# Kernel optimization log

Measured on AMD Instinct MI355X. Metric: run time of the kernel, lower is better.

## Reference

```python
import jax, jax.numpy as jnp
import numpy as np
from jax import lax

RADIUS = 0.1
K_LOCAL = 32
N_CENTROIDS = 2048


def farthest_point_sample(pos, m):
    # Greedy FPS, deterministic start at index 0 (torch version uses a random start).
    pos = lax.stop_gradient(pos)  # index selection is non-differentiable
    N = pos.shape[0]
    big = jnp.finfo(pos.dtype).max

    def step(carry, _):
        dist, current = carry
        d2 = jnp.sum((pos - pos[current]) ** 2, axis=-1)  # (N,)
        dist = jnp.minimum(dist, d2)
        nxt = jnp.argmax(dist).astype(jnp.int32)
        return (dist, nxt), current

    init = (jnp.full((N,), big, dtype=pos.dtype), jnp.int32(0))
    _, idx = lax.scan(step, init, None, length=m)
    return idx  # (m,) int32


def ball_query(pos, centers, radius, k):
    # (M, N) pairwise squared distances -- same dense form as the torch reference.
    d2 = jnp.sum((centers[:, None, :] - pos[None, :, :]) ** 2, axis=-1)
    within = d2 <= radius * radius
    big = jnp.finfo(d2.dtype).max
    masked = jnp.where(within, d2, big)
    _, idx = lax.top_k(-masked, k)              # k smallest distances
    valid = jnp.take_along_axis(within, idx, axis=1)
    fallback = jnp.broadcast_to(idx[:, :1], idx.shape)
    return jnp.where(valid, idx, fallback)      # (M, k) padded with first (nearest) idx


def setup_inputs() -> dict:
    key = jax.random.key(0)
    ks = jax.random.split(key, 5)
    N, C = 50000, 128
    scale = 1.0 / np.sqrt(C)
    return {
        "pos": jax.random.uniform(ks[0], (N, 3), dtype=jnp.float32),
        "feat_scalar": jax.random.normal(ks[1], (N, C, 1), dtype=jnp.float32),
        "feat_vector": jax.random.normal(ks[2], (N, C, 3), dtype=jnp.float32),
        "W_scalar": jax.random.normal(ks[3], (C, C), dtype=jnp.float32) * scale,
        "W_vector": jax.random.normal(ks[4], (C, C), dtype=jnp.float32) * scale,
        "b_scalar": jnp.zeros((C,), dtype=jnp.float32),
        "b_vector": jnp.zeros((C,), dtype=jnp.float32),
    }


def reference(pos, feat_scalar, feat_vector, W_scalar, W_vector, b_scalar, b_vector):
    M = min(N_CENTROIDS, pos.shape[0])
    cent_idx = farthest_point_sample(pos, M)          # (M,)
    centroids = pos[cent_idx]                         # (M, 3)
    nbr_idx = ball_query(pos, centroids, RADIUS, K_LOCAL)  # (M, k)

    def pool_mix(f, W, b):
        f_nbr = f[nbr_idx]                            # (M, k, C, d) gather
        f_pooled = jnp.max(f_nbr, axis=1)             # (M, C, d) max-pool over neighbors
        # ChannelMixer: linear mix across channel dim
        return jnp.einsum('mcd,co->mod', f_pooled, W) + b[None, :, None]

    out_scalar = pool_mix(feat_scalar, W_scalar, b_scalar)
    out_vector = pool_mix(feat_vector, W_vector, b_vector)
    return centroids, out_scalar, out_vector
```

## Files before the change

### kernel.cpp

```cpp
#include <hip/hip_runtime.h>
#include <float.h>

#define N_PTS   50000
#define M_CENT  2048
#define K_LOC   32
#define C_CH    128

typedef unsigned long long u64;
typedef unsigned int u32;

#define FPS_NB   14
#define FPS_NT   512
#define FPS_PPT  7
#define FPS_R    64
#define SLOT_U64 8

__global__ void init_ws_kernel(u64* __restrict__ slots) {
  int t = blockIdx.x * blockDim.x + threadIdx.x;
  if (t < FPS_R * FPS_NB * SLOT_U64) slots[t] = 0ull;
}

template <int CTRL>
__device__ __forceinline__ u32 dppmov_u(u32 v) {
  return (u32)__builtin_amdgcn_update_dpp((int)v, (int)v, CTRL, 0xf, 0xf, false);
}
template <int CTRL>
__device__ __forceinline__ float dppmov_f(float v) {
  return __int_as_float(
      __builtin_amdgcn_update_dpp(__float_as_int(v), __float_as_int(v),
                                  CTRL, 0xf, 0xf, false));
}
__device__ __forceinline__ float wave_max_f32(float v) {
  v = fmaxf(v, dppmov_f<0x111>(v));
  v = fmaxf(v, dppmov_f<0x112>(v));
  v = fmaxf(v, dppmov_f<0x114>(v));
  v = fmaxf(v, dppmov_f<0x118>(v));
  v = fmaxf(v, dppmov_f<0x142>(v));
  v = fmaxf(v, dppmov_f<0x143>(v));
  return __int_as_float(__builtin_amdgcn_readlane(__float_as_int(v), 63));
}
__device__ __forceinline__ u32 wave_max_u32(u32 v) {
  u32 t;
  t = dppmov_u<0x111>(v); v = v > t ? v : t;
  t = dppmov_u<0x112>(v); v = v > t ? v : t;
  t = dppmov_u<0x114>(v); v = v > t ? v : t;
  t = dppmov_u<0x118>(v); v = v > t ? v : t;
  t = dppmov_u<0x142>(v); v = v > t ? v : t;
  t = dppmov_u<0x143>(v); v = v > t ? v : t;
  return (u32)__builtin_amdgcn_readlane((int)v, 63);
}
__device__ __forceinline__ u32 wave_min_u32(u32 v) {
  u32 t;
  t = dppmov_u<0x111>(v); v = v < t ? v : t;
  t = dppmov_u<0x112>(v); v = v < t ? v : t;
  t = dppmov_u<0x114>(v); v = v < t ? v : t;
  t = dppmov_u<0x118>(v); v = v < t ? v : t;
  t = dppmov_u<0x142>(v); v = v < t ? v : t;
  t = dppmov_u<0x143>(v); v = v < t ? v : t;
  return (u32)__builtin_amdgcn_readlane((int)v, 63);
}

__global__ __launch_bounds__(FPS_NT) void fps_kernel(
    const float* __restrict__ pos,
    u64* __restrict__ slots,
    float* __restrict__ cent_out)
{
  const int lane = threadIdx.x & 63;
  const int wv   = threadIdx.x >> 6;
  const int blk  = blockIdx.x;
  const int w    = blk * (FPS_NT/64) + wv;

  float px[FPS_PPT], py[FPS_PPT], pz[FPS_PPT], dist[FPS_PPT];
#pragma unroll
  for (int j = 0; j < FPS_PPT; j++) {
    int n = (w * FPS_PPT + j) * 64 + lane;
    if (n < N_PTS) {
      px[j] = pos[3*n+0]; py[j] = pos[3*n+1]; pz[j] = pos[3*n+2];
      dist[j] = FLT_MAX;
    } else {
      px[j] = 0.f; py[j] = 0.f; pz[j] = 0.f; dist[j] = -1.f;
    }
  }

  __shared__ uint2 s_w[2][FPS_NT/64];
  __shared__ float s_bc[2][3];

  float cx = pos[0], cy = pos[1], cz = pos[2];

  for (int i = 0; i < M_CENT; i++) {
    if (blk == 0 && wv == 0 && lane == 0) {
      cent_out[3*i+0] = cx; cent_out[3*i+1] = cy; cent_out[3*i+2] = cz;
    }
    float lmax = -1.0f;
#pragma unroll
    for (int j = 0; j < FPS_PPT; j++) {
      int n = (w * FPS_PPT + j) * 64 + lane;
      if (n < N_PTS) {
        float dx = __fsub_rn(px[j], cx);
        float dy = __fsub_rn(py[j], cy);
        float dz = __fsub_rn(pz[j], cz);
        float d2 = __fadd_rn(__fadd_rn(__fmul_rn(dx,dx), __fmul_rn(dy,dy)),
                             __fmul_rn(dz,dz));
        float d  = fminf(dist[j], d2);
        dist[j] = d;
        lmax = fmaxf(lmax, d);
      }
    }
    float wmax = wave_max_f32(lmax);
    u32 li = 0xFFFFFFFFu;
#pragma unroll
    for (int j = 0; j < FPS_PPT; j++) {
      int n = (w * FPS_PPT + j) * 64 + lane;
      if (n < N_PTS && dist[j] == wmax) li = li < (u32)n ? li : (u32)n;
    }
    u32 widx = wave_min_u32(li);

    if (i == M_CENT - 1) break;

    if (lane == 0) s_w[i & 1][wv] = make_uint2(__float_as_uint(wmax), widx);
    __syncthreads();

    if (wv == 0) {
      uint2 kv = (lane < FPS_NT/64) ? s_w[i & 1][lane]
                                    : make_uint2(0u, 0xFFFFFFFFu);
      u32 bmaxb = wave_max_u32(kv.x);
      u32 bidx  = wave_min_u32(kv.x == bmaxb ? kv.y : 0xFFFFFFFFu);
      u64* row = slots + (size_t)(i & (FPS_R-1)) * (FPS_NB*SLOT_U64);
      if (lane == 0) {
        u64 key = ((u64)bmaxb << 32) | (u64)(0xFFFFFFFFu - bidx);
        __hip_atomic_store(&row[blk * SLOT_U64], key,
                           __ATOMIC_RELAXED, __HIP_MEMORY_SCOPE_AGENT);
        if (i >= 2)
          __hip_atomic_store(&slots[(size_t)((i-2) & (FPS_R-1)) * (FPS_NB*SLOT_U64)
                                    + blk * SLOT_U64],
                             0ull, __ATOMIC_RELAXED, __HIP_MEMORY_SCOPE_AGENT);
      }
      u64 got = (lane < FPS_NB) ? 0ull : 1ull;
      const u64* sl = row + lane * SLOT_U64;
      while (__ballot(got == 0ull)) {
        if (got == 0ull)
          got = __hip_atomic_load(sl, __ATOMIC_RELAXED, __HIP_MEMORY_SCOPE_AGENT);
      }
      u32 hi = (u32)(got >> 32), lo = (u32)got;
      u32 ic = 0xFFFFFFFFu - lo;
      float qx = 0.f, qy = 0.f, qz = 0.f;
      if (lane < FPS_NB) { qx = pos[3*ic]; qy = pos[3*ic+1]; qz = pos[3*ic+2]; }

      u32 H  = wave_max_u32(lane < FPS_NB ? hi : 0u);
      u32 LO = wave_max_u32((lane < FPS_NB && hi == H) ? lo : 0u);
      u64 msk = __ballot(lane < FPS_NB && hi == H && lo == LO);
      int L = __ffsll((long long)msk) - 1;
      float ncx = __int_as_float(__builtin_amdgcn_readlane(__float_as_int(qx), L));
      float ncy = __int_as_float(__builtin_amdgcn_readlane(__float_as_int(qy), L));
      float ncz = __int_as_float(__builtin_amdgcn_readlane(__float_as_int(qz), L));
      if (lane == 0) {
        s_bc[i & 1][0] = ncx; s_bc[i & 1][1] = ncy; s_bc[i & 1][2] = ncz;
      }
    }
    __syncthreads();
    cx = s_bc[i & 1][0]; cy = s_bc[i & 1][1]; cz = s_bc[i & 1][2];
  }
}

#define BQ_NT  256
#define BQ_CAP 2048

__global__ __launch_bounds__(BQ_NT) void ballq_kernel(
    const float* __restrict__ pos,
    const float* __restrict__ cent,
    int* __restrict__ nbr,
    int* __restrict__ nsel)
{
  __shared__ float s_d2[BQ_CAP];
  __shared__ int   s_idx[BQ_CAP];
  __shared__ int   s_count;
  __shared__ u64   s_red[BQ_NT/64];
  __shared__ u64   s_win;

  const int m = blockIdx.x, tid = threadIdx.x;
  if (tid == 0) s_count = 0;
  __syncthreads();
  const float cx = cent[3*m+0], cy = cent[3*m+1], cz = cent[3*m+2];

  for (int n = tid; n < N_PTS; n += BQ_NT) {
    float dx = __fsub_rn(cx, pos[3*n+0]);
    float dy = __fsub_rn(cy, pos[3*n+1]);
    float dz = __fsub_rn(cz, pos[3*n+2]);
    float d2 = __fadd_rn(__fadd_rn(__fmul_rn(dx,dx), __fmul_rn(dy,dy)),
                         __fmul_rn(dz,dz));
    if (d2 <= 0.01f) {
      int p = atomicAdd(&s_count, 1);
      if (p < BQ_CAP) { s_d2[p] = d2; s_idx[p] = n; }
    }
  }
  __syncthreads();
  int cnt = s_count; if (cnt > BQ_CAP) cnt = BQ_CAP;
  int ns = cnt < K_LOC ? cnt : K_LOC;

  for (int sel = 0; sel < ns; sel++) {
    u64 best = ~0ull;
    for (int p = tid; p < cnt; p += BQ_NT) {
      u64 pk = ((u64)__float_as_uint(s_d2[p]) << 32) | (u64)(u32)s_idx[p];
      if (pk < best) best = pk;
    }
#pragma unroll
    for (int off = 32; off >= 1; off >>= 1) {
      u64 o = __shfl_down(best, off, 64);
      if (o < best) best = o;
    }
    if ((tid & 63) == 0) s_red[tid >> 6] = best;
    __syncthreads();
    if (tid < 64) {
      best = (tid < BQ_NT/64) ? s_red[tid] : ~0ull;
#pragma unroll
      for (int off = 2; off >= 1; off >>= 1) {
        u64 o = __shfl_down(best, off, 64);
        if (o < best) best = o;
      }
      if (tid == 0) s_win = best;
    }
    __syncthreads();
    int widx = (int)(u32)(s_win & 0xFFFFFFFFull);
    if (tid == 0) nbr[m*K_LOC + sel] = widx;
    for (int p = tid; p < cnt; p += BQ_NT) {
      if (s_idx[p] == widx) s_d2[p] = FLT_MAX;
    }
    __syncthreads();
  }
  if (tid == 0) nsel[m] = ns;
}

__global__ __launch_bounds__(C_CH) void pool_mix_kernel(
    const float* __restrict__ fs,
    const float* __restrict__ fv,
    const float* __restrict__ Ws,
    const float* __restrict__ Wv,
    const float* __restrict__ bs,
    const float* __restrict__ bv,
    const int* __restrict__ nbr,
    const int* __restrict__ nsel,
    float* __restrict__ out_s,
    float* __restrict__ out_v)
{
  __shared__ float ps[C_CH];
  __shared__ float pv[C_CH*3];
  const int m = blockIdx.x, o = threadIdx.x;
  const int ns = nsel[m];
  float mS = -FLT_MAX, m0 = -FLT_MAX, m1 = -FLT_MAX, m2 = -FLT_MAX;
  for (int j = 0; j < ns; j++) {
    int n = nbr[m*K_LOC + j];
    mS = fmaxf(mS, fs[(size_t)n*C_CH + o]);
    const float* r = fv + (size_t)n*(C_CH*3) + 3*o;
    m0 = fmaxf(m0, r[0]); m1 = fmaxf(m1, r[1]); m2 = fmaxf(m2, r[2]);
  }
  ps[o] = mS; pv[3*o+0] = m0; pv[3*o+1] = m1; pv[3*o+2] = m2;
  __syncthreads();
  float aS = bs[o];
  float a0 = bv[o], a1 = bv[o], a2 = bv[o];
  for (int cc = 0; cc < C_CH; cc++) {
    float w1 = Ws[cc*C_CH + o];
    float w2 = Wv[cc*C_CH + o];
    aS = fmaf(ps[cc], w1, aS);
    a0 = fmaf(pv[3*cc+0], w2, a0);
    a1 = fmaf(pv[3*cc+1], w2, a1);
    a2 = fmaf(pv[3*cc+2], w2, a2);
  }
  out_s[(size_t)m*C_CH + o] = aS;
  float* ov = out_v + (size_t)m*(C_CH*3) + 3*o;
  ov[0] = a0; ov[1] = a1; ov[2] = a2;
}

extern "C" void kernel_launch(void* const* d_in, const int* in_sizes, int n_in,
                              void* d_out, int out_size, void* d_ws, size_t ws_size,
                              hipStream_t stream) {
  (void)in_sizes; (void)n_in; (void)out_size; (void)ws_size;
  const float* pos = (const float*)d_in[0];
  const float* fs  = (const float*)d_in[1];
  const float* fv  = (const float*)d_in[2];
  const float* Ws  = (const float*)d_in[3];
  const float* Wv  = (const float*)d_in[4];
  const float* bs  = (const float*)d_in[5];
  const float* bv  = (const float*)d_in[6];

  float* out      = (float*)d_out;
  float* cent_out = out;
  float* out_s    = out + 3*M_CENT;
  float* out_v    = out + 3*M_CENT + M_CENT*C_CH;

  char* ws = (char*)d_ws;
  u64* slots = (u64*)ws;
  size_t slots_bytes = (size_t)FPS_R * FPS_NB * SLOT_U64 * 8;
  int* nbr   = (int*)(ws + slots_bytes);
  int* nsel  = (int*)(ws + slots_bytes + (size_t)M_CENT*K_LOC*4);

  init_ws_kernel<<<(FPS_R*FPS_NB*SLOT_U64 + 255)/256, 256, 0, stream>>>(slots);
  fps_kernel<<<FPS_NB, FPS_NT, 0, stream>>>(pos, slots, cent_out);
  ballq_kernel<<<M_CENT, BQ_NT, 0, stream>>>(pos, cent_out, nbr, nsel);
  pool_mix_kernel<<<M_CENT, C_CH, 0, stream>>>(fs, fv, Ws, Wv, bs, bv,
                                               nbr, nsel, out_s, out_v);
}
```

Before: 4.078 ms.

## Co-locate FPS blocks on one XCC and poll slots via L2 atomics

Launches 128 blocks and uses per-XCC tickets so the first XCC to gather 14 blocks wins. Only those 14 run FPS, which keeps all inter-block slot traffic inside one XCC's L2. Because the blocks share an L2, slot loads and stores become non-coherent L2 atomics (atomic_or with sc0, atomic_swap) instead of agent-scope atomics, with a handshake that falls back to the safe path if the blocks cannot all see each other. This is meant to cut the per-iteration cross-block sync latency of the 2048-step FPS loop. In exchange it adds a startup handshake, a bounded-poll escape, and reliance on hardware-specific XCC_ID behaviour. The slot rows 61-63 that the handshake reuses overlap the ring buffer and are not cleared per iteration.

Measured after the change: 3.858 ms. -5.4%, faster.

```diff
diff --git a/kernel.cpp b/kernel.cpp
--- a/kernel.cpp
+++ b/kernel.cpp
@@ -9,15 +9,39 @@
 typedef unsigned long long u64;
 typedef unsigned int u32;
 
-#define FPS_NB   14
-#define FPS_NT   512
-#define FPS_PPT  7
-#define FPS_R    64
-#define SLOT_U64 8
+#define FPS_NB    14
+#define FPS_GRID  128
+#define FPS_NT    512
+#define FPS_PPT   7
+#define FPS_R     64
+#define SLOT_U64  8
+#define ROW_U64   (FPS_NB*SLOT_U64)
+#define FPS_POLL_BOUND (1<<16)
 
 __global__ void init_ws_kernel(u64* __restrict__ slots) {
   int t = blockIdx.x * blockDim.x + threadIdx.x;
   if (t < FPS_R * FPS_NB * SLOT_U64) slots[t] = 0ull;
+}
+
+__device__ __forceinline__ u64 l2a_load(u64* p) {
+  u64 old;
+  asm volatile("global_atomic_or_x2 %0, %1, %2, off sc0\n\ts_waitcnt vmcnt(0)"
+               : "=&v"(old) : "v"(p), "v"(0ull) : "memory");
+  return old;
+}
+__device__ __forceinline__ void l2a_store(u64* p, u64 v) {
+  asm volatile("global_atomic_swap_x2 %0, %1, off"
+               :: "v"(p), "v"(v) : "memory");
+}
+template <bool SAFE>
+__device__ __forceinline__ u64 slot_load(u64* p) {
+  if (SAFE) return __hip_atomic_load(p, __ATOMIC_RELAXED, __HIP_MEMORY_SCOPE_AGENT);
+  return l2a_load(p);
+}
+template <bool SAFE>
+__device__ __forceinline__ void slot_store(u64* p, u64 v) {
+  if (SAFE) __hip_atomic_store(p, v, __ATOMIC_RELAXED, __HIP_MEMORY_SCOPE_AGENT);
+  else      l2a_store(p, v);
 }
 
 template <int CTRL>
@@ -60,15 +84,15 @@
   return (u32)__builtin_amdgcn_readlane((int)v, 63);
 }
 
-__global__ __launch_bounds__(FPS_NT) void fps_kernel(
-    const float* __restrict__ pos,
-    u64* __restrict__ slots,
-    float* __restrict__ cent_out)
+template <bool SAFE>
+__device__ __forceinline__ void fps_main(
+    const float* __restrict__ pos, u64* __restrict__ slots,
+    float* __restrict__ cent_out, const int wid,
+    uint2 (*s_w)[FPS_NT/64], float (*s_bc)[3])
 {
   const int lane = threadIdx.x & 63;
   const int wv   = threadIdx.x >> 6;
-  const int blk  = blockIdx.x;
-  const int w    = blk * (FPS_NT/64) + wv;
+  const int w    = wid * (FPS_NT/64) + wv;
 
   float px[FPS_PPT], py[FPS_PPT], pz[FPS_PPT], dist[FPS_PPT];
 #pragma unroll
@@ -82,13 +106,12 @@
     }
   }
 
-  __shared__ uint2 s_w[2][FPS_NT/64];
-  __shared__ float s_bc[2][3];
+  bool broken = false;
 
   float cx = pos[0], cy = pos[1], cz = pos[2];
 
   for (int i = 0; i < M_CENT; i++) {
-    if (blk == 0 && wv == 0 && lane == 0) {
+    if (wid == 0 && wv == 0 && lane == 0) {
       cent_out[3*i+0] = cx; cent_out[3*i+1] = cy; cent_out[3*i+2] = cz;
     }
     float lmax = -1.0f;
@@ -125,24 +148,35 @@
                                     : make_uint2(0u, 0xFFFFFFFFu);
       u32 bmaxb = wave_max_u32(kv.x);
       u32 bidx  = wave_min_u32(kv.x == bmaxb ? kv.y : 0xFFFFFFFFu);
-      u64* row = slots + (size_t)(i & (FPS_R-1)) * (FPS_NB*SLOT_U64);
-      if (lane == 0) {
-        u64 key = ((u64)bmaxb << 32) | (u64)(0xFFFFFFFFu - bidx);
-        __hip_atomic_store(&row[blk * SLOT_U64], key,
-                           __ATOMIC_RELAXED, __HIP_MEMORY_SCOPE_AGENT);
-        if (i >= 2)
-          __hip_atomic_store(&slots[(size_t)((i-2) & (FPS_R-1)) * (FPS_NB*SLOT_U64)
-                                    + blk * SLOT_U64],
-                             0ull, __ATOMIC_RELAXED, __HIP_MEMORY_SCOPE_AGENT);
-      }
-      u64 got = (lane < FPS_NB) ? 0ull : 1ull;
-      const u64* sl = row + lane * SLOT_U64;
-      while (__ballot(got == 0ull)) {
-        if (got == 0ull)
-          got = __hip_atomic_load(sl, __ATOMIC_RELAXED, __HIP_MEMORY_SCOPE_AGENT);
+      u64 ownkey = ((u64)bmaxb << 32) | (u64)(0xFFFFFFFFu - bidx);
+      u64* row = slots + (size_t)(i & (FPS_R-1)) * ROW_U64;
+
+      u64 got;
+      if (!SAFE && broken) {
+        got = (lane == wid) ? ownkey : 1ull;
+      } else {
+        if (lane == 0) {
+          slot_store<SAFE>(&row[wid * SLOT_U64], ownkey);
+          if (i >= 2)
+            slot_store<SAFE>(&slots[(size_t)((i-2) & (FPS_R-1)) * ROW_U64
+                                    + wid * SLOT_U64], 0ull);
+        }
+        got = (lane < FPS_NB) ? 0ull : 1ull;
+        u64* sl = row + lane * SLOT_U64;
+        int trips = 0;
+        while (__ballot(got == 0ull)) {
+          if (got == 0ull) got = slot_load<SAFE>(sl);
+          if (!SAFE) {
+            if (++trips > FPS_POLL_BOUND) {
+              if (got == 0ull) got = 1ull;
+              broken = true;
+            }
+          }
+        }
       }
       u32 hi = (u32)(got >> 32), lo = (u32)got;
       u32 ic = 0xFFFFFFFFu - lo;
+      if (ic >= N_PTS) ic = 0;
       float qx = 0.f, qy = 0.f, qz = 0.f;
       if (lane < FPS_NB) { qx = pos[3*ic]; qy = pos[3*ic+1]; qz = pos[3*ic+2]; }
 
@@ -160,6 +194,72 @@
     __syncthreads();
     cx = s_bc[i & 1][0]; cy = s_bc[i & 1][1]; cz = s_bc[i & 1][2];
   }
+}
+
+__global__ __launch_bounds__(FPS_NT) void fps_kernel(
+    const float* __restrict__ pos,
+    u64* __restrict__ slots,
+    float* __restrict__ cent_out)
+{
+  __shared__ uint2 s_w[2][FPS_NT/64];
+  __shared__ float s_bc[2][3];
+  __shared__ int   s_role[2];
+
+  if (threadIdx.x == 0) {
+    u32 xcc;
+    asm volatile("s_getreg_b32 %0, hwreg(HW_REG_XCC_ID, 0, 4)" : "=s"(xcc));
+    xcc &= 7u;
+    u64* cntp = slots + 63*ROW_U64 + (size_t)xcc * SLOT_U64 + 1;
+    u64* winp = slots + 63*ROW_U64 + 8 * SLOT_U64 + 1;
+    u64 t = __hip_atomic_fetch_add(cntp, 1ull, __ATOMIC_RELAXED,
+                                   __HIP_MEMORY_SCOPE_AGENT);
+    int ticket = (int)t;
+    if (ticket == FPS_NB - 1) {
+      u64 exp = 0ull;
+      __hip_atomic_compare_exchange_strong(winp, &exp, (u64)(xcc + 1),
+          __ATOMIC_RELAXED, __ATOMIC_RELAXED, __HIP_MEMORY_SCOPE_AGENT);
+    }
+    int role = -1, safe = 0;
+    if (ticket < FPS_NB) {
+      u64 win;
+      do {
+        win = __hip_atomic_load(winp, __ATOMIC_RELAXED, __HIP_MEMORY_SCOPE_AGENT);
+        if (win == 0ull) __builtin_amdgcn_s_sleep(1);
+      } while (win == 0ull);
+      if (win == (u64)(xcc + 1)) {
+        role = ticket;
+        u64* hs = slots + 61*ROW_U64;
+        l2a_store(hs + (size_t)role * SLOT_U64 + 1, 1ull);
+        bool okk = false;
+        for (int trip = 0; trip < 512 && !okk; ++trip) {
+          int seen = 0;
+          for (int j = 0; j < FPS_NB; ++j)
+            seen += (l2a_load(hs + (size_t)j * SLOT_U64 + 1) != 0ull);
+          okk = (seen == FPS_NB);
+          if (!okk) __builtin_amdgcn_s_sleep(8);
+        }
+        u64* okp = slots + 62*ROW_U64;
+        __hip_atomic_store(okp + (size_t)role * SLOT_U64 + 1,
+                           okk ? 2ull : 1ull,
+                           __ATOMIC_RELAXED, __HIP_MEMORY_SCOPE_AGENT);
+        for (int j = 0; j < FPS_NB; ++j) {
+          u64 v;
+          do {
+            v = __hip_atomic_load(okp + (size_t)j * SLOT_U64 + 1,
+                                  __ATOMIC_RELAXED, __HIP_MEMORY_SCOPE_AGENT);
+            if (v == 0ull) __builtin_amdgcn_s_sleep(1);
+          } while (v == 0ull);
+          if (v == 1ull) safe = 1;
+        }
+      }
+    }
+    s_role[0] = role; s_role[1] = safe;
+  }
+  __syncthreads();
+  const int wid = s_role[0];
+  if (wid < 0) return;
+  if (s_role[1]) fps_main<true >(pos, slots, cent_out, wid, s_w, s_bc);
+  else           fps_main<false>(pos, slots, cent_out, wid, s_w, s_bc);
 }
 
 #define BQ_NT  256
@@ -294,7 +394,7 @@
   int* nsel  = (int*)(ws + slots_bytes + (size_t)M_CENT*K_LOC*4);
 
   init_ws_kernel<<<(FPS_R*FPS_NB*SLOT_U64 + 255)/256, 256, 0, stream>>>(slots);
-  fps_kernel<<<FPS_NB, FPS_NT, 0, stream>>>(pos, slots, cent_out);
+  fps_kernel<<<FPS_GRID, FPS_NT, 0, stream>>>(pos, slots, cent_out);
   ballq_kernel<<<M_CENT, BQ_NT, 0, stream>>>(pos, cent_out, nbr, nsel);
   pool_mix_kernel<<<M_CENT, C_CH, 0, stream>>>(fs, fv, Ws, Wv, bs, bv,
                                                nbr, nsel, out_s, out_v);
```

## Replace multi-block FPS with single-block grid-culled FPS using chunk bounding boxes

Applied to the files above, without the earlier changes.

Points are binned into a 10x10x10 grid and sorted into 64-point chunks, each with a bounding box. Farthest point sampling then runs in one 1024-thread block, which replaces the cross-block atomic slot handshake. Each iteration updates only the chunks whose box could still be lowered by the new centroid, since their cached max distance exceeds the lower bound. This cuts per-iteration distance work and global synchronization, at the cost of several preprocessing kernels, global-memory distance reads and writes, and running on a single CU.

After: 4.855 ms. 19.1% more time.

```diff
diff --git a/kernel.cpp b/kernel.cpp
--- a/kernel.cpp
+++ b/kernel.cpp
@@ -9,15 +9,21 @@
 typedef unsigned long long u64;
 typedef unsigned int u32;
 
-#define FPS_NB   14
-#define FPS_NT   512
-#define FPS_PPT  7
-#define FPS_R    64
-#define SLOT_U64 8
-
-__global__ void init_ws_kernel(u64* __restrict__ slots) {
-  int t = blockIdx.x * blockDim.x + threadIdx.x;
-  if (t < FPS_R * FPS_NB * SLOT_U64) slots[t] = 0ull;
+#define G_DIM   10
+#define N_CELL  (G_DIM*G_DIM*G_DIM)
+#define NC_MAX  2048
+#define NP_PAD  50176
+#define FPS1_NT 1024
+#define NWAVE   (FPS1_NT/64)
+
+__device__ __forceinline__ int cell_of(float x, float y, float z) {
+  int a = (int)(x * (float)G_DIM);
+  int b = (int)(y * (float)G_DIM);
+  int c = (int)(z * (float)G_DIM);
+  a = a < 0 ? 0 : (a > G_DIM-1 ? G_DIM-1 : a);
+  b = b < 0 ? 0 : (b > G_DIM-1 ? G_DIM-1 : b);
+  c = c < 0 ? 0 : (c > G_DIM-1 ? G_DIM-1 : c);
+  return (a * G_DIM + b) * G_DIM + c;
 }
 
 template <int CTRL>
@@ -39,126 +45,218 @@
   v = fmaxf(v, dppmov_f<0x143>(v));
   return __int_as_float(__builtin_amdgcn_readlane(__float_as_int(v), 63));
 }
-__device__ __forceinline__ u32 wave_max_u32(u32 v) {
-  u32 t;
-  t = dppmov_u<0x111>(v); v = v > t ? v : t;
-  t = dppmov_u<0x112>(v); v = v > t ? v : t;
-  t = dppmov_u<0x114>(v); v = v > t ? v : t;
-  t = dppmov_u<0x118>(v); v = v > t ? v : t;
-  t = dppmov_u<0x142>(v); v = v > t ? v : t;
-  t = dppmov_u<0x143>(v); v = v > t ? v : t;
-  return (u32)__builtin_amdgcn_readlane((int)v, 63);
-}
-__device__ __forceinline__ u32 wave_min_u32(u32 v) {
-  u32 t;
-  t = dppmov_u<0x111>(v); v = v < t ? v : t;
-  t = dppmov_u<0x112>(v); v = v < t ? v : t;
-  t = dppmov_u<0x114>(v); v = v < t ? v : t;
-  t = dppmov_u<0x118>(v); v = v < t ? v : t;
-  t = dppmov_u<0x142>(v); v = v < t ? v : t;
-  t = dppmov_u<0x143>(v); v = v < t ? v : t;
-  return (u32)__builtin_amdgcn_readlane((int)v, 63);
-}
-
-__global__ __launch_bounds__(FPS_NT) void fps_kernel(
+__device__ __forceinline__ float wave_min_f32(float v) {
+  v = fminf(v, dppmov_f<0x111>(v));
+  v = fminf(v, dppmov_f<0x112>(v));
+  v = fminf(v, dppmov_f<0x114>(v));
+  v = fminf(v, dppmov_f<0x118>(v));
+  v = fminf(v, dppmov_f<0x142>(v));
+  v = fminf(v, dppmov_f<0x143>(v));
+  return __int_as_float(__builtin_amdgcn_readlane(__float_as_int(v), 63));
+}
+template <int CTRL>
+__device__ __forceinline__ u64 dpp_u64(u64 v) {
+  u32 hi = dppmov_u<CTRL>((u32)(v >> 32));
+  u32 lo = dppmov_u<CTRL>((u32)v);
+  return ((u64)hi << 32) | (u64)lo;
+}
+__device__ __forceinline__ u64 wave_max_u64(u64 v) {
+  u64 t;
+  t = dpp_u64<0x111>(v); if (t > v) v = t;
+  t = dpp_u64<0x112>(v); if (t > v) v = t;
+  t = dpp_u64<0x114>(v); if (t > v) v = t;
+  t = dpp_u64<0x118>(v); if (t > v) v = t;
+  t = dpp_u64<0x142>(v); if (t > v) v = t;
+  t = dpp_u64<0x143>(v); if (t > v) v = t;
+  u32 rh = (u32)__builtin_amdgcn_readlane((int)(v >> 32), 63);
+  u32 rl = (u32)__builtin_amdgcn_readlane((int)(v & 0xFFFFFFFFull), 63);
+  return ((u64)rh << 32) | (u64)rl;
+}
+
+__global__ void init_zero_kernel(int* __restrict__ p, int n) {
+  int t = blockIdx.x * blockDim.x + threadIdx.x;
+  if (t < n) p[t] = 0;
+}
+
+__global__ void hist_kernel(const float* __restrict__ pos,
+                            int* __restrict__ cellcnt) {
+  int n = blockIdx.x * blockDim.x + threadIdx.x;
+  if (n >= N_PTS) return;
+  atomicAdd(&cellcnt[cell_of(pos[3*n], pos[3*n+1], pos[3*n+2])], 1);
+}
+
+__global__ __launch_bounds__(1024) void scan_kernel(
+    const int* __restrict__ cellcnt, int* __restrict__ cursor,
+    int2* __restrict__ rng, int* __restrict__ ncp)
+{
+  __shared__ int s[1024];
+  const int tid = threadIdx.x;
+  int cnt = (tid < N_CELL) ? cellcnt[tid] : 0;
+  s[tid] = cnt;
+  __syncthreads();
+  for (int off = 1; off < 1024; off <<= 1) {
+    int add = (tid >= off) ? s[tid - off] : 0;
+    __syncthreads();
+    s[tid] += add;
+    __syncthreads();
+  }
+  int pofs = s[tid] - cnt;
+  int nch  = (cnt + 63) >> 6;
+  __syncthreads();
+  s[tid] = nch;
+  __syncthreads();
+  for (int off = 1; off < 1024; off <<= 1) {
+    int add = (tid >= off) ? s[tid - off] : 0;
+    __syncthreads();
+    s[tid] += add;
+    __syncthreads();
+  }
+  int chbase = s[tid] - nch;
+  if (tid < N_CELL) {
+    cursor[tid] = pofs;
+    for (int k = 0; k < nch; k++) {
+      int rem = cnt - (k << 6);
+      rng[chbase + k] = make_int2(pofs + (k << 6), rem < 64 ? rem : 64);
+    }
+  }
+  if (tid == 1023) *ncp = s[1023];
+}
+
+__global__ void scatter_kernel(const float* __restrict__ pos,
+    int* __restrict__ cursor,
+    float* __restrict__ spx, float* __restrict__ spy,
+    float* __restrict__ spz, int* __restrict__ sidx)
+{
+  int n = blockIdx.x * blockDim.x + threadIdx.x;
+  if (n >= N_PTS) return;
+  float x = pos[3*n], y = pos[3*n+1], z = pos[3*n+2];
+  int p = atomicAdd(&cursor[cell_of(x, y, z)], 1);
+  spx[p] = x; spy[p] = y; spz[p] = z; sidx[p] = n;
+}
+
+__global__ __launch_bounds__(64) void bbox_kernel(
+    const float* __restrict__ spx, const float* __restrict__ spy,
+    const float* __restrict__ spz, const int2* __restrict__ rng,
+    const int* __restrict__ ncp,
+    float4* __restrict__ bb_lo, float4* __restrict__ bb_hi,
+    float* __restrict__ sdist)
+{
+  const int b = blockIdx.x, lane = threadIdx.x;
+  int gid = b * 64 + lane;
+  if (gid < N_PTS) sdist[gid] = FLT_MAX;
+  int NC = *ncp;
+  if (b >= NC) return;
+  int2 rc = rng[b];
+  bool v = lane < rc.y;
+  int g = rc.x + lane;
+  float x = v ? spx[g] : 0.f, y = v ? spy[g] : 0.f, z = v ? spz[g] : 0.f;
+  float lx = wave_min_f32(v ? x :  FLT_MAX);
+  float ly = wave_min_f32(v ? y :  FLT_MAX);
+  float lz = wave_min_f32(v ? z :  FLT_MAX);
+  float hx = wave_max_f32(v ? x : -FLT_MAX);
+  float hy = wave_max_f32(v ? y : -FLT_MAX);
+  float hz = wave_max_f32(v ? z : -FLT_MAX);
+  if (lane == 0) {
+    bb_lo[b] = make_float4(lx, ly, lz, 0.f);
+    bb_hi[b] = make_float4(hx, hy, hz, 0.f);
+  }
+}
+
+__global__ __launch_bounds__(FPS1_NT) void fps_kernel(
     const float* __restrict__ pos,
-    u64* __restrict__ slots,
-    float* __restrict__ cent_out)
-{
-  const int lane = threadIdx.x & 63;
-  const int wv   = threadIdx.x >> 6;
-  const int blk  = blockIdx.x;
-  const int w    = blk * (FPS_NT/64) + wv;
-
-  float px[FPS_PPT], py[FPS_PPT], pz[FPS_PPT], dist[FPS_PPT];
-#pragma unroll
-  for (int j = 0; j < FPS_PPT; j++) {
-    int n = (w * FPS_PPT + j) * 64 + lane;
-    if (n < N_PTS) {
-      px[j] = pos[3*n+0]; py[j] = pos[3*n+1]; pz[j] = pos[3*n+2];
-      dist[j] = FLT_MAX;
-    } else {
-      px[j] = 0.f; py[j] = 0.f; pz[j] = 0.f; dist[j] = -1.f;
-    }
-  }
-
-  __shared__ uint2 s_w[2][FPS_NT/64];
-  __shared__ float s_bc[2][3];
+    const float* __restrict__ spx, const float* __restrict__ spy,
+    const float* __restrict__ spz, const int* __restrict__ sidx,
+    float* __restrict__ sdist, const int2* __restrict__ rng,
+    const float4* __restrict__ bb_lo, const float4* __restrict__ bb_hi,
+    const int* __restrict__ ncp, float* __restrict__ cent_out)
+{
+  __shared__ u64  l_key[NC_MAX];
+  __shared__ int2 l_rng[NC_MAX];
+  __shared__ int  l_act[NC_MAX];
+  __shared__ u64  l_red[NWAVE];
+  __shared__ int  l_nact;
+  __shared__ u32  l_win;
+
+  const int tid = threadIdx.x, lane = tid & 63, wv = tid >> 6;
+  const int NC = *ncp;
+
+  for (int c = tid; c < NC; c += FPS1_NT) {
+    l_rng[c] = rng[c];
+    l_key[c] = ((u64)0x7F7FFFFFu) << 32;
+  }
+  __syncthreads();
 
   float cx = pos[0], cy = pos[1], cz = pos[2];
 
   for (int i = 0; i < M_CENT; i++) {
-    if (blk == 0 && wv == 0 && lane == 0) {
+    if (tid == 0) {
       cent_out[3*i+0] = cx; cent_out[3*i+1] = cy; cent_out[3*i+2] = cz;
-    }
-    float lmax = -1.0f;
-#pragma unroll
-    for (int j = 0; j < FPS_PPT; j++) {
-      int n = (w * FPS_PPT + j) * 64 + lane;
-      if (n < N_PTS) {
-        float dx = __fsub_rn(px[j], cx);
-        float dy = __fsub_rn(py[j], cy);
-        float dz = __fsub_rn(pz[j], cz);
-        float d2 = __fadd_rn(__fadd_rn(__fmul_rn(dx,dx), __fmul_rn(dy,dy)),
-                             __fmul_rn(dz,dz));
-        float d  = fminf(dist[j], d2);
-        dist[j] = d;
-        lmax = fmaxf(lmax, d);
+      l_nact = 0;
+    }
+    if (i == M_CENT - 1) break;
+    __syncthreads();
+
+    for (int c0 = 0; c0 < NC; c0 += FPS1_NT) {
+      int c = c0 + tid;
+      bool act = false;
+      if (c < NC) {
+        float cmax = __uint_as_float((u32)(l_key[c] >> 32));
+        float4 lo = bb_lo[c], hi = bb_hi[c];
+        float ax = fmaxf(fmaxf(__fsub_rn(lo.x, cx), __fsub_rn(cx, hi.x)), 0.f);
+        float ay = fmaxf(fmaxf(__fsub_rn(lo.y, cy), __fsub_rn(cy, hi.y)), 0.f);
+        float az = fmaxf(fmaxf(__fsub_rn(lo.z, cz), __fsub_rn(cz, hi.z)), 0.f);
+        float LB = (ax*ax + ay*ay + az*az) * 0.999f;
+        act = LB < cmax;
       }
-    }
-    float wmax = wave_max_f32(lmax);
-    u32 li = 0xFFFFFFFFu;
-#pragma unroll
-    for (int j = 0; j < FPS_PPT; j++) {
-      int n = (w * FPS_PPT + j) * 64 + lane;
-      if (n < N_PTS && dist[j] == wmax) li = li < (u32)n ? li : (u32)n;
-    }
-    u32 widx = wave_min_u32(li);
-
-    if (i == M_CENT - 1) break;
-
-    if (lane == 0) s_w[i & 1][wv] = make_uint2(__float_as_uint(wmax), widx);
-    __syncthreads();
-
+      u64 m = __ballot(act);
+      if (m) {
+        int leader = __ffsll((long long)m) - 1;
+        int base = 0;
+        if (lane == leader) base = atomicAdd(&l_nact, __popcll(m));
+        base = __shfl(base, leader, 64);
+        if (act)
+          l_act[base + __popcll(m & ((1ull << lane) - 1ull))] = c;
+      }
+    }
+    __syncthreads();
+
+    int nact = l_nact;
+    for (int a = wv; a < nact; a += NWAVE) {
+      int c = l_act[a];
+      int2 rc = l_rng[c];
+      u64 key = 0ull;
+      if (lane < rc.y) {
+        int g = rc.x + lane;
+        float dx = __fsub_rn(spx[g], cx);
+        float dy = __fsub_rn(spy[g], cy);
+        float dz = __fsub_rn(spz[g], cz);
+        float d2 = __fadd_rn(__fadd_rn(__fmul_rn(dx, dx), __fmul_rn(dy, dy)),
+                             __fmul_rn(dz, dz));
+        float d = fminf(sdist[g], d2);
+        sdist[g] = d;
+        key = ((u64)__float_as_uint(d) << 32) | (u64)(u32)(~(u32)sidx[g]);
+      }
+      key = wave_max_u64(key);
+      if (lane == 0) l_key[c] = key;
+    }
+    __syncthreads();
+
+    u64 best = 0ull;
+    for (int c = tid; c < NC; c += FPS1_NT) {
+      u64 k = l_key[c];
+      if (k > best) best = k;
+    }
+    best = wave_max_u64(best);
+    if (lane == 0) l_red[wv] = best;
+    __syncthreads();
     if (wv == 0) {
-      uint2 kv = (lane < FPS_NT/64) ? s_w[i & 1][lane]
-                                    : make_uint2(0u, 0xFFFFFFFFu);
-      u32 bmaxb = wave_max_u32(kv.x);
-      u32 bidx  = wave_min_u32(kv.x == bmaxb ? kv.y : 0xFFFFFFFFu);
-      u64* row = slots + (size_t)(i & (FPS_R-1)) * (FPS_NB*SLOT_U64);
-      if (lane == 0) {
-        u64 key = ((u64)bmaxb << 32) | (u64)(0xFFFFFFFFu - bidx);
-        __hip_atomic_store(&row[blk * SLOT_U64], key,
-                           __ATOMIC_RELAXED, __HIP_MEMORY_SCOPE_AGENT);
-        if (i >= 2)
-          __hip_atomic_store(&slots[(size_t)((i-2) & (FPS_R-1)) * (FPS_NB*SLOT_U64)
-                                    + blk * SLOT_U64],
-                             0ull, __ATOMIC_RELAXED, __HIP_MEMORY_SCOPE_AGENT);
-      }
-      u64 got = (lane < FPS_NB) ? 0ull : 1ull;
-      const u64* sl = row + lane * SLOT_U64;
-      while (__ballot(got == 0ull)) {
-        if (got == 0ull)
-          got = __hip_atomic_load(sl, __ATOMIC_RELAXED, __HIP_MEMORY_SCOPE_AGENT);
-      }
-      u32 hi = (u32)(got >> 32), lo = (u32)got;
-      u32 ic = 0xFFFFFFFFu - lo;
-      float qx = 0.f, qy = 0.f, qz = 0.f;
-      if (lane < FPS_NB) { qx = pos[3*ic]; qy = pos[3*ic+1]; qz = pos[3*ic+2]; }
-
-      u32 H  = wave_max_u32(lane < FPS_NB ? hi : 0u);
-      u32 LO = wave_max_u32((lane < FPS_NB && hi == H) ? lo : 0u);
-      u64 msk = __ballot(lane < FPS_NB && hi == H && lo == LO);
-      int L = __ffsll((long long)msk) - 1;
-      float ncx = __int_as_float(__builtin_amdgcn_readlane(__float_as_int(qx), L));
-      float ncy = __int_as_float(__builtin_amdgcn_readlane(__float_as_int(qy), L));
-      float ncz = __int_as_float(__builtin_amdgcn_readlane(__float_as_int(qz), L));
-      if (lane == 0) {
-        s_bc[i & 1][0] = ncx; s_bc[i & 1][1] = ncy; s_bc[i & 1][2] = ncz;
-      }
-    }
-    __syncthreads();
-    cx = s_bc[i & 1][0]; cy = s_bc[i & 1][1]; cz = s_bc[i & 1][2];
+      u64 b = (lane < NWAVE) ? l_red[lane] : 0ull;
+      b = wave_max_u64(b);
+      if (lane == 0) l_win = ~(u32)(b & 0xFFFFFFFFull);
+    }
+    __syncthreads();
+    u32 widx = l_win;
+    cx = pos[3*widx+0]; cy = pos[3*widx+1]; cz = pos[3*widx+2];
   }
 }
 
@@ -288,13 +386,30 @@
   float* out_v    = out + 3*M_CENT + M_CENT*C_CH;
 
   char* ws = (char*)d_ws;
-  u64* slots = (u64*)ws;
-  size_t slots_bytes = (size_t)FPS_R * FPS_NB * SLOT_U64 * 8;
-  int* nbr   = (int*)(ws + slots_bytes);
-  int* nsel  = (int*)(ws + slots_bytes + (size_t)M_CENT*K_LOC*4);
-
-  init_ws_kernel<<<(FPS_R*FPS_NB*SLOT_U64 + 255)/256, 256, 0, stream>>>(slots);
-  fps_kernel<<<FPS_NB, FPS_NT, 0, stream>>>(pos, slots, cent_out);
+  size_t off = 0;
+  float* spx   = (float*)(ws + off); off += (size_t)NP_PAD * 4;
+  float* spy   = (float*)(ws + off); off += (size_t)NP_PAD * 4;
+  float* spz   = (float*)(ws + off); off += (size_t)NP_PAD * 4;
+  int*   sidx  = (int*)  (ws + off); off += (size_t)NP_PAD * 4;
+  float* sdist = (float*)(ws + off); off += (size_t)NP_PAD * 4;
+  int*   cellcnt = (int*)(ws + off); off += 1024 * 4;
+  int*   cursor  = (int*)(ws + off); off += 1024 * 4;
+  int*   ncp     = (int*)(ws + off); off += 256;
+  int2*  rng     = (int2*)(ws + off); off += (size_t)NC_MAX * 8;
+  float4* bb_lo  = (float4*)(ws + off); off += (size_t)NC_MAX * 16;
+  float4* bb_hi  = (float4*)(ws + off); off += (size_t)NC_MAX * 16;
+  int*   nbr     = (int*)(ws + off); off += (size_t)M_CENT * K_LOC * 4;
+  int*   nsel    = (int*)(ws + off); off += (size_t)M_CENT * 4;
+
+  init_zero_kernel<<<(2112 + 255)/256, 256, 0, stream>>>(cellcnt, 2112);
+  hist_kernel<<<(N_PTS + 255)/256, 256, 0, stream>>>(pos, cellcnt);
+  scan_kernel<<<1, 1024, 0, stream>>>(cellcnt, cursor, rng, ncp);
+  scatter_kernel<<<(N_PTS + 255)/256, 256, 0, stream>>>(pos, cursor,
+                                                        spx, spy, spz, sidx);
+  bbox_kernel<<<NC_MAX, 64, 0, stream>>>(spx, spy, spz, rng, ncp,
+                                         bb_lo, bb_hi, sdist);
+  fps_kernel<<<1, FPS1_NT, 0, stream>>>(pos, spx, spy, spz, sidx, sdist,
+                                        rng, bb_lo, bb_hi, ncp, cent_out);
   ballq_kernel<<<M_CENT, BQ_NT, 0, stream>>>(pos, cent_out, nbr, nsel);
   pool_mix_kernel<<<M_CENT, C_CH, 0, stream>>>(fs, fv, Ws, Wv, bs, bv,
                                                nbr, nsel, out_s, out_v);
```
